# Kernel optimization log

Hardware: AMD Instinct MI355X
Metric: run time of the kernel (lower is better)

## Reference

```python
import jax, jax.numpy as jnp
import numpy as np

N = 50000
E = 800000
IN_DIM = 256
HID = 64
HEADS = 4
OUT_DIM = 32
NEG_SLOPE = 0.2


def gat_conv(x, edge_index, W, a_src, a_dst, bias, heads, out_ch, concat):
    """PyG-style GATConv (eval mode, add_self_loops=True).
    x: [N, F_in]; edge_index: [2, E'] with row0=src, row1=dst.
    W: [F_in, heads*out_ch]; a_src/a_dst: [heads, out_ch]; bias: [heads*out_ch] or [out_ch].
    """
    n = x.shape[0]
    # add self loops
    loops = jnp.arange(n, dtype=edge_index.dtype)
    src = jnp.concatenate([edge_index[0], loops])
    dst = jnp.concatenate([edge_index[1], loops])

    h = (x @ W).reshape(n, heads, out_ch)              # [N, H, C]
    alpha_s = jnp.einsum('nhc,hc->nh', h, a_src)       # [N, H]
    alpha_d = jnp.einsum('nhc,hc->nh', h, a_dst)       # [N, H]
    e = alpha_s[src] + alpha_d[dst]                    # [E', H]
    e = jnp.where(e >= 0, e, NEG_SLOPE * e)            # leaky_relu

    # segment softmax over incoming edges of each dst node
    m = jax.ops.segment_max(e, dst, num_segments=n)    # [N, H]
    ex = jnp.exp(e - m[dst])
    denom = jax.ops.segment_sum(ex, dst, num_segments=n)
    alpha = ex / (denom[dst] + 1e-16)                  # [E', H]

    msg = h[src] * alpha[:, :, None]                   # [E', H, C]
    out = jax.ops.segment_sum(msg, dst, num_segments=n)  # [N, H, C]
    out = out.reshape(n, heads * out_ch) if concat else out.mean(axis=1)
    return out + bias


def setup_inputs() -> dict:
    key = jax.random.key(0)
    ks = jax.random.split(key, 10)
    x = jax.random.normal(ks[0], (N, IN_DIM), dtype=jnp.float32)
    edge_index = jax.random.randint(ks[1], (2, E), 0, N, dtype=jnp.int32)
    s1 = 1.0 / np.sqrt(IN_DIM)
    s2 = 1.0 / np.sqrt(HEADS * HID)
    return {
        'x': x,
        'edge_index': edge_index,
        'W1': jax.random.normal(ks[2], (IN_DIM, HEADS * HID), dtype=jnp.float32) * s1,
        'a_src1': jax.random.normal(ks[3], (HEADS, HID), dtype=jnp.float32) * s2,
        'a_dst1': jax.random.normal(ks[4], (HEADS, HID), dtype=jnp.float32) * s2,
        'b1': jnp.zeros((HEADS * HID,), dtype=jnp.float32),
        'W2': jax.random.normal(ks[5], (HEADS * HID, OUT_DIM), dtype=jnp.float32) * s2,
        'a_src2': jax.random.normal(ks[6], (1, OUT_DIM), dtype=jnp.float32) * 0.125,
        'a_dst2': jax.random.normal(ks[7], (1, OUT_DIM), dtype=jnp.float32) * 0.125,
        'b2': jnp.zeros((OUT_DIM,), dtype=jnp.float32),
    }


def reference(x, edge_index, W1, a_src1, a_dst1, b1, W2, a_src2, a_dst2, b2):
    h = gat_conv(x, edge_index, W1, a_src1, a_dst1, b1, HEADS, HID, concat=True)
    h = jax.nn.elu(h)
    out = gat_conv(h, edge_index, W2, a_src2, a_dst2, b2, 1, OUT_DIM, concat=False)
    return out
```

## Files before the change

kernel.cpp:

```cpp
#include <hip/hip_runtime.h>

#define NEG_SLOPE 0.2f
#define CAP 64
#define LOG2E 1.44269504f

typedef short bf16x8 __attribute__((ext_vector_type(8)));
typedef float f32x4 __attribute__((ext_vector_type(4)));
typedef _Float16 half2v __attribute__((ext_vector_type(2)));
typedef _Float16 half4v __attribute__((ext_vector_type(4)));
typedef _Float16 half8v __attribute__((ext_vector_type(8)));

__device__ inline short bf16_rne(float x) {
    unsigned u = __float_as_uint(x);
    unsigned r = u + 0x7FFFu + ((u >> 16) & 1u);
    return (short)(r >> 16);
}

__device__ inline float fast_exp2(float x) {
#if __has_builtin(__builtin_amdgcn_exp2f)
    return __builtin_amdgcn_exp2f(x);
#else
    return exp2f(x);
#endif
}


__global__ void k_prepw(const float* __restrict__ W1, short* __restrict__ Wt,
                        const float* __restrict__ W2, _Float16* __restrict__ W2t,
                        int* __restrict__ cursor, int* __restrict__ col, int N) {
    int colc = blockIdx.x;
    int k = threadIdx.x;
    Wt[(size_t)colc * 256 + k] = bf16_rne(W1[(size_t)k * 256 + colc]);
    if (colc < 32) W2t[(size_t)colc * 256 + k] = (_Float16)W2[(size_t)k * 32 + colc];
    int gid = blockIdx.x * 256 + threadIdx.x;
    if (gid < N) {
        cursor[gid] = 1;
        col[(size_t)gid * CAP] = gid;
    }
}


__global__ void k_scatter(const int* __restrict__ src, const int* __restrict__ dst,
                          int* cursor, int* col, int E) {
    int i = blockIdx.x * 256 + threadIdx.x;
    if (i < E) {
        int d = dst[i];
        int p = atomicAdd(&cursor[d], 1);
        if (p < CAP) col[(size_t)d * CAP + p] = src[i];
    }
}


__global__ __launch_bounds__(256) void k_gemm1(
        const float* __restrict__ x, const short* __restrict__ Wt,
        const float* __restrict__ a_src, const float* __restrict__ a_dst,
        _Float16* __restrict__ h1, float* __restrict__ as1, float* __restrict__ ad1, int N) {
    __shared__ short Ab[64 * 40];
    __shared__ short Bb[256 * 40];
    const int tid = threadIdx.x;
    const int lane = tid & 63;
    const int wc = tid >> 6;
    const int row0 = blockIdx.x * 64;
    const int m15 = lane & 15, quad = lane >> 4;

    f32x4 acc[4][4] = {};

    const int arow = tid >> 2;
    const int akseg = (tid & 3) * 8;

    for (int k0 = 0; k0 < 256; k0 += 32) {
        {
            int row = row0 + arow;
            float vals[8];
            if (row < N) {
                float4 v0 = *(const float4*)(x + (size_t)row * 256 + k0 + akseg);
                float4 v1 = *(const float4*)(x + (size_t)row * 256 + k0 + akseg + 4);
                vals[0] = v0.x; vals[1] = v0.y; vals[2] = v0.z; vals[3] = v0.w;
                vals[4] = v1.x; vals[5] = v1.y; vals[6] = v1.z; vals[7] = v1.w;
            } else {
#pragma unroll
                for (int i = 0; i < 8; ++i) vals[i] = 0.f;
            }
            short buf[8];
#pragma unroll
            for (int i = 0; i < 8; ++i) buf[i] = bf16_rne(vals[i]);
            *(bf16x8*)&Ab[arow * 40 + akseg] = *(bf16x8*)&buf[0];
        }
        {
#pragma unroll
            for (int s = 0; s < 4; ++s)
                *(bf16x8*)&Bb[tid * 40 + s * 8] =
                    *(const bf16x8*)(Wt + (size_t)tid * 256 + k0 + s * 8);
        }
        __syncthreads();
        bf16x8 ab[4];
#pragma unroll
        for (int mt = 0; mt < 4; ++mt)
            ab[mt] = *(const bf16x8*)&Ab[(mt * 16 + m15) * 40 + quad * 8];
#pragma unroll
        for (int nt = 0; nt < 4; ++nt) {
            int nn = wc * 64 + nt * 16 + m15;
            bf16x8 bb = *(const bf16x8*)&Bb[nn * 40 + quad * 8];
#pragma unroll
            for (int mt = 0; mt < 4; ++mt)
                acc[mt][nt] = __builtin_amdgcn_mfma_f32_16x16x32_bf16(ab[mt], bb, acc[mt][nt], 0, 0, 0);
        }
        __syncthreads();
    }
    const int head = wc;
#pragma unroll
    for (int mt = 0; mt < 4; ++mt) {
        float va[4] = {0.f, 0.f, 0.f, 0.f};
        float vd[4] = {0.f, 0.f, 0.f, 0.f};
#pragma unroll
        for (int nt = 0; nt < 4; ++nt) {
            int colg = wc * 64 + nt * 16 + m15;
            float asv = a_src[colg];
            float adv = a_dst[colg];
#pragma unroll
            for (int r = 0; r < 4; ++r) {
                float accv = acc[mt][nt][r];
                int row = row0 + mt * 16 + quad * 4 + r;
                if (row < N) h1[(size_t)row * 256 + colg] = (_Float16)accv;
                va[r] = fmaf(accv, asv, va[r]);
                vd[r] = fmaf(accv, adv, vd[r]);
            }
        }
#pragma unroll
        for (int r = 0; r < 4; ++r) {
#pragma unroll
            for (int mq = 1; mq < 16; mq <<= 1) {
                va[r] += __shfl_xor(va[r], mq);
                vd[r] += __shfl_xor(vd[r], mq);
            }
            int row = row0 + mt * 16 + quad * 4 + r;
            if (m15 == 0 && row < N) {
                as1[(size_t)row * 4 + head] = va[r] * LOG2E;
                ad1[(size_t)row * 4 + head] = vd[r] * LOG2E;
            }
        }
    }
}


__global__ __launch_bounds__(256) void k_fuse1(
        const _Float16* __restrict__ h1, const float* __restrict__ as1,
        const float* __restrict__ ad1, const int* __restrict__ cursor,
        const int* __restrict__ col, const float* __restrict__ b1,
        const _Float16* __restrict__ W2t, const float* __restrict__ a_s2,
        const float* __restrict__ a_d2, _Float16* __restrict__ z,
        float* __restrict__ as2, float* __restrict__ ad2, int N) {
    __shared__ _Float16 W2s[32 * 264];
    __shared__ _Float16 h2s[4 * 256];
    const int tid = threadIdx.x;
    const int l = tid & 63;
    const int wave = tid >> 6;
    const int n = blockIdx.x * 4 + wave;

    for (int i8 = tid; i8 < 1024; i8 += 256) {
        int elem = i8 * 8;
        int row = elem >> 8, k = elem & 255;
        *(half8v*)&W2s[row * 264 + k] = *(const half8v*)(W2t + (size_t)row * 256 + k);
    }
    __syncthreads();
    if (n >= N) return;

    const int head = l >> 4;
    const int beg = n * CAP;
    int deg = __builtin_amdgcn_readfirstlane(cursor[n]);
    if (deg > CAP) deg = CAP;
    int colv = (l < deg) ? col[beg + l] : 0;
    float adv = ad1[(size_t)n * 4 + head];

    f32x4 a0 = {}, a1 = {}, a2 = {}, a3 = {};
    float s0 = 0.f, s1 = 0.f, s2 = 0.f, s3 = 0.f;
    int j = 0;
    for (; j + 3 < deg; j += 4) {
        int c0 = __builtin_amdgcn_readlane(colv, j);
        int c1 = __builtin_amdgcn_readlane(colv, j + 1);
        int c2 = __builtin_amdgcn_readlane(colv, j + 2);
        int c3 = __builtin_amdgcn_readlane(colv, j + 3);
        float e0 = as1[(size_t)c0 * 4 + head] + adv;
        float e1 = as1[(size_t)c1 * 4 + head] + adv;
        float e2 = as1[(size_t)c2 * 4 + head] + adv;
        float e3 = as1[(size_t)c3 * 4 + head] + adv;
        e0 = fmaxf(e0, NEG_SLOPE * e0); e1 = fmaxf(e1, NEG_SLOPE * e1);
        e2 = fmaxf(e2, NEG_SLOPE * e2); e3 = fmaxf(e3, NEG_SLOPE * e3);
        float p0 = fast_exp2(e0), p1 = fast_exp2(e1);
        float p2 = fast_exp2(e2), p3 = fast_exp2(e3);
        half4v h0 = *((const half4v*)(h1 + (size_t)c0 * 256) + l);
        half4v hv1 = *((const half4v*)(h1 + (size_t)c1 * 256) + l);
        half4v h2 = *((const half4v*)(h1 + (size_t)c2 * 256) + l);
        half4v h3 = *((const half4v*)(h1 + (size_t)c3 * 256) + l);
        s0 += p0; s1 += p1; s2 += p2; s3 += p3;
        a0 += __builtin_convertvector(h0, f32x4) * p0;
        a1 += __builtin_convertvector(hv1, f32x4) * p1;
        a2 += __builtin_convertvector(h2, f32x4) * p2;
        a3 += __builtin_convertvector(h3, f32x4) * p3;
    }
    for (; j < deg; ++j) {
        int c0 = __builtin_amdgcn_readlane(colv, j);
        float e0 = as1[(size_t)c0 * 4 + head] + adv;
        e0 = fmaxf(e0, NEG_SLOPE * e0);
        float p0 = fast_exp2(e0);
        half4v h0 = *((const half4v*)(h1 + (size_t)c0 * 256) + l);
        s0 += p0;
        a0 += __builtin_convertvector(h0, f32x4) * p0;
    }
    f32x4 at = (a0 + a1) + (a2 + a3);
    float iv = 1.f / ((s0 + s1) + (s2 + s3) + 1e-16f);
    float4 bb = *(const float4*)(b1 + l * 4);
    float4 v;
    v.x = at[0] * iv + bb.x;
    v.y = at[1] * iv + bb.y;
    v.z = at[2] * iv + bb.z;
    v.w = at[3] * iv + bb.w;
    v.x = (v.x > 0.f) ? v.x : (__expf(v.x) - 1.f);
    v.y = (v.y > 0.f) ? v.y : (__expf(v.y) - 1.f);
    v.z = (v.z > 0.f) ? v.z : (__expf(v.z) - 1.f);
    v.w = (v.w > 0.f) ? v.w : (__expf(v.w) - 1.f);
    half4v hv;
    hv.x = (_Float16)v.x; hv.y = (_Float16)v.y; hv.z = (_Float16)v.z; hv.w = (_Float16)v.w;
    *((half4v*)(h2s + wave * 256) + l) = hv;

    int c = l & 31;
    int kh = (l >> 5) * 128;
    const _Float16* hrow = h2s + wave * 256 + kh;
    const _Float16* wrow = W2s + c * 264 + kh;
    float accz = 0.f;
#pragma unroll
    for (int k = 0; k < 128; k += 8) {
        half8v hz = *(const half8v*)(hrow + k);
        half8v wz = *(const half8v*)(wrow + k);
#if __has_builtin(__builtin_amdgcn_fdot2)
        accz = __builtin_amdgcn_fdot2(__builtin_shufflevector(hz, hz, 0, 1),
                                      __builtin_shufflevector(wz, wz, 0, 1), accz, false);
        accz = __builtin_amdgcn_fdot2(__builtin_shufflevector(hz, hz, 2, 3),
                                      __builtin_shufflevector(wz, wz, 2, 3), accz, false);
        accz = __builtin_amdgcn_fdot2(__builtin_shufflevector(hz, hz, 4, 5),
                                      __builtin_shufflevector(wz, wz, 4, 5), accz, false);
        accz = __builtin_amdgcn_fdot2(__builtin_shufflevector(hz, hz, 6, 7),
                                      __builtin_shufflevector(wz, wz, 6, 7), accz, false);
#else
        accz = fmaf((float)hz[0], (float)wz[0], accz);
        accz = fmaf((float)hz[1], (float)wz[1], accz);
        accz = fmaf((float)hz[2], (float)wz[2], accz);
        accz = fmaf((float)hz[3], (float)wz[3], accz);
        accz = fmaf((float)hz[4], (float)wz[4], accz);
        accz = fmaf((float)hz[5], (float)wz[5], accz);
        accz = fmaf((float)hz[6], (float)wz[6], accz);
        accz = fmaf((float)hz[7], (float)wz[7], accz);
#endif
    }
    accz += __shfl_xor(accz, 32);
    float za = accz * a_s2[c];
    float zd = accz * a_d2[c];
#pragma unroll
    for (int mq = 1; mq < 32; mq <<= 1) {
        za += __shfl_xor(za, mq);
        zd += __shfl_xor(zd, mq);
    }
    if (l < 32) z[(size_t)n * 32 + c] = (_Float16)accz;
    if (l == 0) {
        as2[n] = za * LOG2E;
        ad2[n] = zd * LOG2E;
    }
}


__global__ void k_gather2(const _Float16* __restrict__ z, const float* __restrict__ as2,
                          const float* __restrict__ ad2, const int* __restrict__ cursor,
                          const int* __restrict__ col, const float* __restrict__ b2,
                          float* __restrict__ out, int N) {
    int n = blockIdx.x * 4 + (threadIdx.x >> 6);
    if (n >= N) return;
    int l = threadIdx.x & 63;
    int eo = l >> 3;
    int cg = l & 7;
    int beg = n * CAP;
    int deg = __builtin_amdgcn_readfirstlane(cursor[n]);
    if (deg > CAP) deg = CAP;
    int colv = (l < deg) ? col[beg + l] : 0;
    float adn = ad2[n];
    f32x4 acc = {};
    float s = 0.f;
    for (int j0 = 0; j0 < deg; j0 += 8) {
        int jl = j0 + eo;
        bool valid = jl < deg;
        int jc = valid ? jl : deg - 1;
        int src = __shfl(colv, jc);
        float e = as2[src] + adn;
        e = fmaxf(e, NEG_SLOPE * e);
        float p = valid ? fast_exp2(e) : 0.f;
        half4v zv = *((const half4v*)(z + (size_t)src * 32) + cg);
        s += p;
        acc += __builtin_convertvector(zv, f32x4) * p;
    }
    float ax = acc[0], ay = acc[1], az = acc[2], aw = acc[3];
#pragma unroll
    for (int mq = 8; mq < 64; mq <<= 1) {
        ax += __shfl_xor(ax, mq);
        ay += __shfl_xor(ay, mq);
        az += __shfl_xor(az, mq);
        aw += __shfl_xor(aw, mq);
        s += __shfl_xor(s, mq);
    }
    if (eo == 0) {
        float iv = 1.f / (s + 1e-16f);
        float4 bb = *(const float4*)(b2 + cg * 4);
        float4 v;
        v.x = ax * iv + bb.x;
        v.y = ay * iv + bb.y;
        v.z = az * iv + bb.z;
        v.w = aw * iv + bb.w;
        *(float4*)(out + (size_t)n * 32 + cg * 4) = v;
    }
}


extern "C" void kernel_launch(void* const* d_in, const int* in_sizes, int n_in,
                              void* d_out, int out_size, void* d_ws, size_t ws_size,
                              hipStream_t stream) {
    const float* x    = (const float*)d_in[0];
    const int*   ei   = (const int*)d_in[1];
    const float* W1   = (const float*)d_in[2];
    const float* a_s1 = (const float*)d_in[3];
    const float* a_d1 = (const float*)d_in[4];
    const float* b1   = (const float*)d_in[5];
    const float* W2   = (const float*)d_in[6];
    const float* a_s2 = (const float*)d_in[7];
    const float* a_d2 = (const float*)d_in[8];
    const float* b2   = (const float*)d_in[9];
    float* out = (float*)d_out;

    const int N = in_sizes[0] / 256;
    const int E = in_sizes[1] / 2;
    const int* srcIdx = ei;
    const int* dstIdx = ei + E;

    char* ws = (char*)d_ws;
    size_t off = 0;
    auto alloc = [&](size_t bytes) {
        void* p = ws + off;
        off += (bytes + 255) & ~(size_t)255;
        return p;
    };
    _Float16* h1   = (_Float16*)alloc((size_t)N * 256 * 2);
    _Float16* z    = (_Float16*)alloc((size_t)N * 32 * 2);
    float* as1    = (float*)alloc((size_t)N * 16);
    float* ad1    = (float*)alloc((size_t)N * 16);
    float* as2    = (float*)alloc((size_t)N * 4);
    float* ad2    = (float*)alloc((size_t)N * 4);
    short* Wt     = (short*)alloc((size_t)256 * 256 * 2);
    _Float16* W2t = (_Float16*)alloc((size_t)32 * 256 * 2);
    int*   cursor = (int*)alloc((size_t)N * 4);
    int*   col    = (int*)alloc((size_t)N * CAP * 4);

    k_prepw<<<256, 256, 0, stream>>>(W1, Wt, W2, W2t, cursor, col, N);
    k_scatter<<<(E + 255) / 256, 256, 0, stream>>>(srcIdx, dstIdx, cursor, col, E);

    k_gemm1<<<(N + 63) / 64, 256, 0, stream>>>(x, Wt, a_s1, a_d1, h1, as1, ad1, N);

    k_fuse1<<<(N + 3) / 4, 256, 0, stream>>>(h1, as1, ad1, cursor, col, b1, W2t,
                                             a_s2, a_d2, z, as2, ad2, N);

    k_gather2<<<(N + 3) / 4, 256, 0, stream>>>(z, as2, ad2, cursor, col, b2, out, N);
}
```

Before: 261.7 us.

## Merge edge scatter into GEMM launch and software-pipeline layer-2 gather loads

The edge-bucketing scatter kernel is folded into the first GEMM kernel as extra trailing blocks, so the scatter's atomics run alongside the GEMM tiles instead of as a separate launch. Separately, the layer-2 gather loop now prefetches the next step's neighbor index, attention score and feature vector before working on the current one, to hide gather latency. The merged kernel declares large shared arrays, which may reduce occupancy for the scatter blocks, and the prefetch uses more registers.

Measured after the change: 262.0 us. About the same (+0.1%).

```diff
diff --git a/kernel.cpp b/kernel.cpp
--- a/kernel.cpp
+++ b/kernel.cpp
@@ -40,23 +40,26 @@
 }
 
 
-__global__ void k_scatter(const int* __restrict__ src, const int* __restrict__ dst,
-                          int* cursor, int* col, int E) {
-    int i = blockIdx.x * 256 + threadIdx.x;
-    if (i < E) {
-        int d = dst[i];
-        int p = atomicAdd(&cursor[d], 1);
-        if (p < CAP) col[(size_t)d * CAP + p] = src[i];
-    }
-}
-
-
-__global__ __launch_bounds__(256) void k_gemm1(
+__global__ __launch_bounds__(256) void k_gemm_scatter(
         const float* __restrict__ x, const short* __restrict__ Wt,
         const float* __restrict__ a_src, const float* __restrict__ a_dst,
-        _Float16* __restrict__ h1, float* __restrict__ as1, float* __restrict__ ad1, int N) {
+        _Float16* __restrict__ h1, float* __restrict__ as1, float* __restrict__ ad1,
+        int N, int nGemm,
+        const int* __restrict__ srcI, const int* __restrict__ dstI,
+        int* __restrict__ cursor, int* __restrict__ col, int E) {
     __shared__ short Ab[64 * 40];
     __shared__ short Bb[256 * 40];
+
+    if ((int)blockIdx.x >= nGemm) {
+        int i = ((int)blockIdx.x - nGemm) * 256 + threadIdx.x;
+        if (i < E) {
+            int d = dstI[i];
+            int p = atomicAdd(&cursor[d], 1);
+            if (p < CAP) col[(size_t)d * CAP + p] = srcI[i];
+        }
+        return;
+    }
+
     const int tid = threadIdx.x;
     const int lane = tid & 63;
     const int wc = tid >> 6;
@@ -169,7 +172,8 @@
     const int beg = n * CAP;
     int deg = __builtin_amdgcn_readfirstlane(cursor[n]);
     if (deg > CAP) deg = CAP;
-    int colv = (l < deg) ? col[beg + l] : 0;
+    int colv = 0;
+    if (l < deg) colv = col[beg + l];
     float adv = ad1[(size_t)n * 4 + head];
 
     f32x4 a0 = {}, a1 = {}, a2 = {}, a3 = {};
@@ -280,21 +284,29 @@
     int beg = n * CAP;
     int deg = __builtin_amdgcn_readfirstlane(cursor[n]);
     if (deg > CAP) deg = CAP;
-    int colv = (l < deg) ? col[beg + l] : 0;
+    int colv = 0;
+    if (l < deg) colv = col[beg + l];
     float adn = ad2[n];
     f32x4 acc = {};
     float s = 0.f;
-    for (int j0 = 0; j0 < deg; j0 += 8) {
-        int jl = j0 + eo;
-        bool valid = jl < deg;
-        int jc = valid ? jl : deg - 1;
-        int src = __shfl(colv, jc);
-        float e = as2[src] + adn;
+
+    const int nst = (deg + 7) >> 3;
+    int srcA = __shfl(colv, eo);
+    float aA = as2[srcA];
+    half4v zA = *((const half4v*)(z + (size_t)srcA * 32) + cg);
+    for (int t = 0; t < nst; ++t) {
+        int srcB = 0; float aB = 0.f; half4v zB = {};
+        if (t + 1 < nst) {
+            srcB = __shfl(colv, (t + 1) * 8 + eo);
+            aB = as2[srcB];
+            zB = *((const half4v*)(z + (size_t)srcB * 32) + cg);
+        }
+        float e = aA + adn;
         e = fmaxf(e, NEG_SLOPE * e);
-        float p = valid ? fast_exp2(e) : 0.f;
-        half4v zv = *((const half4v*)(z + (size_t)src * 32) + cg);
+        float p = (t * 8 + eo < deg) ? fast_exp2(e) : 0.f;
         s += p;
-        acc += __builtin_convertvector(zv, f32x4) * p;
+        acc += __builtin_convertvector(zA, f32x4) * p;
+        srcA = srcB; aA = aB; zA = zB;
     }
     float ax = acc[0], ay = acc[1], az = acc[2], aw = acc[3];
 #pragma unroll
@@ -357,9 +369,11 @@
     int*   col    = (int*)alloc((size_t)N * CAP * 4);
 
     k_prepw<<<256, 256, 0, stream>>>(W1, Wt, W2, W2t, cursor, col, N);
-    k_scatter<<<(E + 255) / 256, 256, 0, stream>>>(srcIdx, dstIdx, cursor, col, E);
-
-    k_gemm1<<<(N + 63) / 64, 256, 0, stream>>>(x, Wt, a_s1, a_d1, h1, as1, ad1, N);
+
+    const int nGemm = (N + 63) / 64;
+    const int nScat = (E + 255) / 256;
+    k_gemm_scatter<<<nGemm + nScat, 256, 0, stream>>>(
+        x, Wt, a_s1, a_d1, h1, as1, ad1, N, nGemm, srcIdx, dstIdx, cursor, col, E);
 
     k_fuse1<<<(N + 3) / 4, 256, 0, stream>>>(h1, as1, ad1, cursor, col, b1, W2t,
                                              a_s2, a_d2, z, as2, ad2, N);
```
